# Kernel tuning notes

Measured on AMD Instinct MI355X. Metric: run time of the kernel, lower is better.

## Reference

```python
import jax, jax.numpy as jnp
import numpy as np

N_NODES = 50000
N_EDGES = 1600000
D_IN = 256
HEADS = 4
SUB_IN = 64   # generate_sub_head_nums(256, 4) -> [64, 64, 64, 64]
SUB_H = 64    # hidden_dim // head_num


def setup_inputs() -> dict:
    key = jax.random.key(0)
    k1, k2, k3 = jax.random.split(key, 3)
    x = jax.random.normal(k1, (N_NODES, D_IN), dtype=jnp.float32)
    edge_index = jax.random.randint(k2, (2, N_EDGES), 0, N_NODES, dtype=jnp.int64)
    # per-head GCNConv weights: glorot-ish scale
    W = jax.random.normal(k3, (HEADS, SUB_IN, SUB_H), dtype=jnp.float32) * (1.0 / np.sqrt(SUB_IN))
    b = jnp.zeros((HEADS, SUB_H), dtype=jnp.float32)
    return {"x": x, "edge_index": edge_index, "W": W, "b": b}


def _gcn_aggregate(x_sub, edge_index, n_nodes):
    """Symmetric-normalized aggregation with self-loops: D^-1/2 (A+I) D^-1/2 x_sub."""
    row, col = edge_index[0], edge_index[1]          # source -> target
    loops = jnp.arange(n_nodes, dtype=row.dtype)
    row2 = jnp.concatenate([row, loops])
    col2 = jnp.concatenate([col, loops])
    deg = jax.ops.segment_sum(jnp.ones_like(col2, dtype=x_sub.dtype), col2,
                              num_segments=n_nodes)
    dinv = jnp.where(deg > 0, jax.lax.rsqrt(deg), 0.0)
    norm = dinv[row2] * dinv[col2]                   # [E+N]
    msgs = x_sub[row2] * norm[:, None]               # [E+N, SUB_IN] gather
    return jax.ops.segment_sum(msgs, col2, num_segments=n_nodes)  # [N, SUB_IN] scatter


def reference(x, edge_index, W, b):
    n = x.shape[0]
    # Faithful to source bug: `start` never advances, so every head reads x[:, 0:SUB_IN].
    x0 = x[:, :SUB_IN]                               # [N, 64], shared by all heads
    # aggregation is linear -> aggregate once, then apply per-head linear (same math as GCNConv(xW))
    agg = _gcn_aggregate(x0, edge_index, n)          # [N, 64]
    heads = jax.nn.relu(jnp.einsum('nf,hfo->nho', agg, W) + b[None, :, :])  # [N, H, SUB_H]
    x_cat = heads.reshape(n, HEADS * SUB_H)          # concat over heads along last dim
    return x_cat, heads
```

## Files before the change

kernel.cpp:

```cpp
#include <hip/hip_runtime.h>
#include <hip/hip_bf16.h>

#define NNODES 50000
#define NEDGES 1600000
#define NBIN   782
#define CAPB   2880
#define BCHUNK 2000
#define NBBLK  800
#define BCPAD  16

__device__ __forceinline__ float bf2f(unsigned short u) {
    union { unsigned int i; float f; } x; x.i = ((unsigned int)u) << 16; return x.f;
}

__global__ __launch_bounds__(256) void k_bin(const int* __restrict__ edges,
                                             int* __restrict__ bincur,
                                             int* __restrict__ binned) {
    __shared__ int pk[BCHUNK];
    __shared__ int hist[NBIN];
    __shared__ int gbase[NBIN];
    __shared__ int lcnt[NBIN];
    int t = threadIdx.x;
    int e0 = blockIdx.x * BCHUNK;
    for (int i = t; i < NBIN; i += 256) { hist[i] = 0; lcnt[i] = 0; }
    __syncthreads();
    for (int i = t * 4; i < BCHUNK; i += 1024) {
        int4 r4 = *(const int4*)&edges[e0 + i];
        int4 c4 = *(const int4*)&edges[NEDGES + e0 + i];
        int b0 = c4.x >> 6, b1 = c4.y >> 6, b2 = c4.z >> 6, b3 = c4.w >> 6;
        pk[i + 0] = r4.x | ((c4.x & 63) << 16) | (b0 << 22);
        pk[i + 1] = r4.y | ((c4.y & 63) << 16) | (b1 << 22);
        pk[i + 2] = r4.z | ((c4.z & 63) << 16) | (b2 << 22);
        pk[i + 3] = r4.w | ((c4.w & 63) << 16) | (b3 << 22);
        atomicAdd(&hist[b0], 1);
        atomicAdd(&hist[b1], 1);
        atomicAdd(&hist[b2], 1);
        atomicAdd(&hist[b3], 1);
    }
    __syncthreads();
    for (int i = t; i < NBIN; i += 256) {
        int h = hist[i];
        gbase[i] = (h > 0) ? atomicAdd(&bincur[i * BCPAD], h) : 0;
    }
    __syncthreads();
    for (int i = t; i < BCHUNK; i += 256) {
        int v = pk[i];
        int bin = ((unsigned)v) >> 22;
        int p = gbase[bin] + atomicAdd(&lcnt[bin], 1);
        if (p < CAPB) binned[bin * CAPB + p] = v & 0x3FFFFF;
    }
}

__global__ __launch_bounds__(256) void k_sortbin(const int* __restrict__ bincur,
                                                 const int* __restrict__ binned,
                                                 const float* __restrict__ x,
                                                 int* __restrict__ rowptr,
                                                 int* __restrict__ cntn,
                                                 float* __restrict__ dinv,
                                                 unsigned short* __restrict__ x0s,
                                                 int* __restrict__ csr) {
    __shared__ int h[64];
    __shared__ int off[64];
    __shared__ int cur[64];
    __shared__ float dv[64];
    __shared__ int stage[CAPB];
    int t = threadIdx.x, bin = blockIdx.x;
    int wave = t >> 6, lane = t & 63;
    if (t < 64) h[t] = 0;
    __syncthreads();
    int len = min(bincur[bin * BCPAD], CAPB);
    const int* __restrict__ bb = binned + bin * CAPB;
    for (int e = t; e < len; e += 256)
        atomicAdd(&h[bb[e] >> 16], 1);
    __syncthreads();
    if (t == 0) {
        int s = 0;
        for (int i = 0; i < 64; ++i) { off[i] = s; cur[i] = s; s += h[i]; }
    }
    __syncthreads();
    if (t < 64) {
        int n = bin * 64 + t;
        float dc = rsqrtf((float)(h[t] + 1));
        dv[t] = dc;
        if (n < NNODES) {
            dinv[n] = dc;
            rowptr[n] = bin * CAPB + off[t];
            cntn[n] = h[t];
        }
    }
    __syncthreads();
    for (int e = t; e < len; e += 256) {
        int v = bb[e];
        int p = atomicAdd(&cur[v >> 16], 1);
        stage[p] = v & 0xFFFF;
    }
    __syncthreads();
    for (int e = t; e < len; e += 256)
        csr[bin * CAPB + e] = stage[e];
    for (int i = wave; i < 64; i += 4) {
        int n = bin * 64 + i;
        if (n < NNODES) {
            __hip_bfloat16 v = __float2bfloat16(x[n * 256 + lane] * dv[i]);
            x0s[n * 64 + lane] = *(unsigned short*)&v;
        }
    }
}

__global__ __launch_bounds__(256) void k_gather(const unsigned short* __restrict__ x0s,
                                                const int* __restrict__ rowptr,
                                                const int* __restrict__ cntn,
                                                const float* __restrict__ dinv,
                                                const int* __restrict__ csr,
                                                float* __restrict__ agg) {
    int wave = threadIdx.x >> 6, lane = threadIdx.x & 63;
    int n = blockIdx.x * 4 + wave;
    int start = rowptr[n], len = cntn[n];
    float acc0 = bf2f(x0s[n * 64 + lane]);
    float acc1 = 0.0f;
    for (int base = 0; base < len; base += 64) {
        int m = min(len - base, 64);
        int idx = (lane < m) ? csr[start + base + lane] : 0;
        int j = 0;
        for (; j + 8 <= m; j += 8) {
            int r0 = __shfl(idx, j + 0), r1 = __shfl(idx, j + 1);
            int r2 = __shfl(idx, j + 2), r3 = __shfl(idx, j + 3);
            int r4 = __shfl(idx, j + 4), r5 = __shfl(idx, j + 5);
            int r6 = __shfl(idx, j + 6), r7 = __shfl(idx, j + 7);
            float f0 = bf2f(x0s[r0 * 64 + lane]);
            float f1 = bf2f(x0s[r1 * 64 + lane]);
            float f2 = bf2f(x0s[r2 * 64 + lane]);
            float f3 = bf2f(x0s[r3 * 64 + lane]);
            float f4 = bf2f(x0s[r4 * 64 + lane]);
            float f5 = bf2f(x0s[r5 * 64 + lane]);
            float f6 = bf2f(x0s[r6 * 64 + lane]);
            float f7 = bf2f(x0s[r7 * 64 + lane]);
            acc0 += (f0 + f1) + (f2 + f3);
            acc1 += (f4 + f5) + (f6 + f7);
        }
        for (; j < m; ++j) {
            int r = __shfl(idx, j);
            acc0 += bf2f(x0s[r * 64 + lane]);
        }
    }
    agg[n * 64 + lane] = (acc0 + acc1) * dinv[n];
}

__global__ __launch_bounds__(256) void k_gemm(const float* __restrict__ agg,
                                              const float* __restrict__ W,
                                              const float* __restrict__ b,
                                              float* __restrict__ out0,
                                              float* __restrict__ out1) {
    int t = threadIdx.x;
    int h = t >> 6, o = t & 63;
    float wreg[64];
    #pragma unroll
    for (int f = 0; f < 64; ++f) wreg[f] = W[h * 4096 + f * 64 + o];
    float bias = b[t];
    int n0 = blockIdx.x * 8;
    for (int i = 0; i < 8; ++i) {
        int n = n0 + i;
        const float* __restrict__ arow = agg + n * 64;
        float acc = bias;
        #pragma unroll
        for (int f = 0; f < 64; ++f) acc = fmaf(arow[f], wreg[f], acc);
        float v = fmaxf(acc, 0.0f);
        __builtin_nontemporal_store(v, &out0[n * 256 + t]);
        __builtin_nontemporal_store(v, &out1[n * 256 + t]);
    }
}


extern "C" void kernel_launch(void* const* d_in, const int* in_sizes, int n_in,
                              void* d_out, int out_size, void* d_ws, size_t ws_size,
                              hipStream_t stream) {
    const float* x     = (const float*)d_in[0];
    const int*   edges = (const int*)d_in[1];
    const float* W     = (const float*)d_in[2];
    const float* b     = (const float*)d_in[3];

    float* out0 = (float*)d_out;
    float* out1 = out0 + (size_t)NNODES * 256;

    char* ws = (char*)d_ws;
    int*            bincur = (int*)(ws + 0);
    float*          dinv   = (float*)(ws + 50176);
    int*            rowptr = (int*)(ws + 250368);
    int*            cntn   = (int*)(ws + 450560);
    int*            binned = (int*)(ws + 650752);
    int*            csr    = (int*)(ws + 9659392);
    unsigned short* x0s    = (unsigned short*)(ws + 18668032);
    float*          agg    = (float*)(ws + 25068032);

    hipMemsetAsync(bincur, 0, NBIN * BCPAD * sizeof(int), stream);
    k_bin    <<<NBBLK, 256, 0, stream>>>(edges, bincur, binned);
    k_sortbin<<<NBIN, 256, 0, stream>>>(bincur, binned, x, rowptr, cntn, dinv, x0s, csr);
    k_gather <<<NNODES / 4, 256, 0, stream>>>(x0s, rowptr, cntn, dinv, csr, agg);
    k_gemm   <<<NNODES / 8, 256, 0, stream>>>(agg, W, b, out0, out1);
}
```

Measured before the change: 273.3 us.

## Shard bin counters per XCD with overflow list to cut cross-die atomics

```diff
diff --git a/kernel.cpp b/kernel.cpp
--- a/kernel.cpp
+++ b/kernel.cpp
@@ -5,9 +5,10 @@
 #define NEDGES 1600000
 #define NBIN   782
 #define CAPB   2880
+#define SCAP   512
+#define OVFCAP 65536
 #define BCHUNK 2000
 #define NBBLK  800
-#define BCPAD  16
 
 __device__ __forceinline__ float bf2f(unsigned short u) {
     union { unsigned int i; float f; } x; x.i = ((unsigned int)u) << 16; return x.f;
@@ -15,6 +16,8 @@
 
 __global__ __launch_bounds__(256) void k_bin(const int* __restrict__ edges,
                                              int* __restrict__ bincur,
+                                             int* __restrict__ ovfcnt,
+                                             int* __restrict__ ovf,
                                              int* __restrict__ binned) {
     __shared__ int pk[BCHUNK];
     __shared__ int hist[NBIN];
@@ -22,6 +25,9 @@
     __shared__ int lcnt[NBIN];
     int t = threadIdx.x;
     int e0 = blockIdx.x * BCHUNK;
+    unsigned xcd;
+    asm volatile("s_getreg_b32 %0, hwreg(HW_REG_XCC_ID)" : "=s"(xcd));
+    xcd &= 7;
     for (int i = t; i < NBIN; i += 256) { hist[i] = 0; lcnt[i] = 0; }
     __syncthreads();
     for (int i = t * 4; i < BCHUNK; i += 1024) {
@@ -40,19 +46,26 @@
     __syncthreads();
     for (int i = t; i < NBIN; i += 256) {
         int h = hist[i];
-        gbase[i] = (h > 0) ? atomicAdd(&bincur[i * BCPAD], h) : 0;
+        gbase[i] = (h > 0) ? atomicAdd(&bincur[xcd * NBIN + i], h) : 0;
     }
     __syncthreads();
     for (int i = t; i < BCHUNK; i += 256) {
         int v = pk[i];
         int bin = ((unsigned)v) >> 22;
         int p = gbase[bin] + atomicAdd(&lcnt[bin], 1);
-        if (p < CAPB) binned[bin * CAPB + p] = v & 0x3FFFFF;
+        if (p < SCAP) {
+            binned[(xcd * NBIN + bin) * SCAP + p] = v & 0x3FFFFF;
+        } else {
+            int op = atomicAdd(ovfcnt, 1);
+            if (op < OVFCAP) ovf[op] = v;
+        }
     }
 }
 
 __global__ __launch_bounds__(256) void k_sortbin(const int* __restrict__ bincur,
                                                  const int* __restrict__ binned,
+                                                 const int* __restrict__ ovfcnt,
+                                                 const int* __restrict__ ovf,
                                                  const float* __restrict__ x,
                                                  int* __restrict__ rowptr,
                                                  int* __restrict__ cntn,
@@ -63,39 +76,65 @@
     __shared__ int off[64];
     __shared__ int cur[64];
     __shared__ float dv[64];
+    __shared__ int slen[8];
     __shared__ int stage[CAPB];
     int t = threadIdx.x, bin = blockIdx.x;
     int wave = t >> 6, lane = t & 63;
     if (t < 64) h[t] = 0;
-    __syncthreads();
-    int len = min(bincur[bin * BCPAD], CAPB);
-    const int* __restrict__ bb = binned + bin * CAPB;
-    for (int e = t; e < len; e += 256)
-        atomicAdd(&h[bb[e] >> 16], 1);
-    __syncthreads();
-    if (t == 0) {
-        int s = 0;
-        for (int i = 0; i < 64; ++i) { off[i] = s; cur[i] = s; s += h[i]; }
+    if (t < 8) slen[t] = min(bincur[t * NBIN + bin], SCAP);
+    __syncthreads();
+    int novf = ovfcnt[0];
+    for (int s = 0; s < 8; ++s) {
+        const int* __restrict__ bb = binned + (s * NBIN + bin) * SCAP;
+        int len = slen[s];
+        for (int e = t; e < len; e += 256)
+            atomicAdd(&h[bb[e] >> 16], 1);
+    }
+    for (int e = t; e < novf; e += 256) {
+        int v = ovf[e];
+        if (((unsigned)v >> 22) == (unsigned)bin) atomicAdd(&h[(v >> 16) & 63], 1);
     }
     __syncthreads();
     if (t < 64) {
+        int v = h[t];
+        int inc = v;
+        #pragma unroll
+        for (int d = 1; d < 64; d <<= 1) {
+            int u = __shfl_up(inc, d);
+            if (lane >= d) inc += u;
+        }
+        int ex = inc - v;
+        off[t] = ex;
+        cur[t] = ex;
+        float dc = rsqrtf((float)(v + 1));
+        dv[t] = dc;
         int n = bin * 64 + t;
-        float dc = rsqrtf((float)(h[t] + 1));
-        dv[t] = dc;
         if (n < NNODES) {
             dinv[n] = dc;
-            rowptr[n] = bin * CAPB + off[t];
-            cntn[n] = h[t];
-        }
-    }
-    __syncthreads();
-    for (int e = t; e < len; e += 256) {
-        int v = bb[e];
-        int p = atomicAdd(&cur[v >> 16], 1);
-        stage[p] = v & 0xFFFF;
-    }
-    __syncthreads();
-    for (int e = t; e < len; e += 256)
+            rowptr[n] = bin * CAPB + ex;
+            cntn[n] = v;
+        }
+    }
+    __syncthreads();
+    for (int s = 0; s < 8; ++s) {
+        const int* __restrict__ bb = binned + (s * NBIN + bin) * SCAP;
+        int len = slen[s];
+        for (int e = t; e < len; e += 256) {
+            int v = bb[e];
+            int p = atomicAdd(&cur[v >> 16], 1);
+            if (p < CAPB) stage[p] = v & 0xFFFF;
+        }
+    }
+    for (int e = t; e < novf; e += 256) {
+        int v = ovf[e];
+        if (((unsigned)v >> 22) == (unsigned)bin) {
+            int p = atomicAdd(&cur[(v >> 16) & 63], 1);
+            if (p < CAPB) stage[p] = v & 0xFFFF;
+        }
+    }
+    __syncthreads();
+    int total = min(off[63] + h[63], CAPB);
+    for (int e = t; e < total; e += 256)
         csr[bin * CAPB + e] = stage[e];
     for (int i = wave; i < 64; i += 4) {
         int n = bin * 64 + i;
@@ -183,17 +222,19 @@
 
     char* ws = (char*)d_ws;
     int*            bincur = (int*)(ws + 0);
-    float*          dinv   = (float*)(ws + 50176);
-    int*            rowptr = (int*)(ws + 250368);
-    int*            cntn   = (int*)(ws + 450560);
-    int*            binned = (int*)(ws + 650752);
-    int*            csr    = (int*)(ws + 9659392);
-    unsigned short* x0s    = (unsigned short*)(ws + 18668032);
-    float*          agg    = (float*)(ws + 25068032);
-
-    hipMemsetAsync(bincur, 0, NBIN * BCPAD * sizeof(int), stream);
-    k_bin    <<<NBBLK, 256, 0, stream>>>(edges, bincur, binned);
-    k_sortbin<<<NBIN, 256, 0, stream>>>(bincur, binned, x, rowptr, cntn, dinv, x0s, csr);
+    int*            ovfcnt = (int*)(ws + 25024);
+    int*            ovf    = (int*)(ws + 25600);
+    float*          dinv   = (float*)(ws + 287744);
+    int*            rowptr = (int*)(ws + 487936);
+    int*            cntn   = (int*)(ws + 688128);
+    int*            binned = (int*)(ws + 888320);
+    int*            csr    = (int*)(ws + 13700608);
+    unsigned short* x0s    = (unsigned short*)(ws + 22709248);
+    float*          agg    = (float*)(ws + 29109248);
+
+    hipMemsetAsync(ws, 0, 25028, stream);
+    k_bin    <<<NBBLK, 256, 0, stream>>>(edges, bincur, ovfcnt, ovf, binned);
+    k_sortbin<<<NBIN, 256, 0, stream>>>(bincur, binned, ovfcnt, ovf, x, rowptr, cntn, dinv, x0s, csr);
     k_gather <<<NNODES / 4, 256, 0, stream>>>(x0s, rowptr, cntn, dinv, csr, agg);
     k_gemm   <<<NNODES / 8, 256, 0, stream>>>(agg, W, b, out0, out1);
 }
```

Measured after the change: 245.6 us. 1.11x faster.
